# Kernel optimization log

Hardware: AMD Instinct MI355X
Metric: run time of the kernel (lower is better)

The kernel has to match this reference:

```python
import jax, jax.numpy as jnp
import numpy as np

B, T, C = 4, 4096, 1024
H, CS = 16, 128
D = C // H
EPS = 1e-5

def _ln(x, g, b):
    m = jnp.mean(x, axis=-1, keepdims=True)
    v = jnp.var(x, axis=-1, keepdims=True)
    return (x - m) * jax.lax.rsqrt(v + EPS) * g + b

def setup_inputs() -> dict:
    key = jax.random.key(0)
    ks = jax.random.split(key, 12)
    s_c = 1.0 / np.sqrt(C)
    s_2d = 1.0 / np.sqrt(2 * D)
    return {
        "x": jax.random.normal(ks[0], (B, T, C), jnp.float32),
        "mark_W": jax.random.normal(ks[1], (C, C), jnp.float32) * s_c,
        "mark_b": jnp.zeros((C,), jnp.float32),
        "gate_W": jax.random.normal(ks[2], (C, C), jnp.float32) * s_c,
        "gate_b": jnp.zeros((C,), jnp.float32),
        "carry_g": jnp.ones((D,), jnp.float32),
        "carry_b": jnp.zeros((D,), jnp.float32),
        "card_g": jnp.ones((D,), jnp.float32),
        "card_b": jnp.zeros((D,), jnp.float32),
        "ho1_W": jax.random.normal(ks[3], (2 * D, 2 * D), jnp.float32) * s_2d,
        "ho1_b": jnp.zeros((2 * D,), jnp.float32),
        "ho2_W": jax.random.normal(ks[4], (2 * D, D), jnp.float32) * s_2d,
        "ho2_b": jnp.zeros((D,), jnp.float32),
        "proj_W": jax.random.normal(ks[5], (C, C), jnp.float32) * s_c * 0.02,
        "proj_b": jnp.zeros((C,), jnp.float32),
        "ln_g": jnp.ones((C,), jnp.float32),
        "ln_b": jnp.zeros((C,), jnp.float32),
    }

def reference(x, mark_W, mark_b, gate_W, gate_b, carry_g, carry_b,
              card_g, card_b, ho1_W, ho1_b, ho2_W, ho2_b,
              proj_W, proj_b, ln_g, ln_b):
    b, t, c = x.shape
    nc = t // CS  # T chosen divisible by chunk_size -> pad_len = 0
    pm = x @ mark_W + mark_b                       # [B,T,C]
    gates = jax.nn.sigmoid(x @ gate_W + gate_b)    # [B,T,C]

    def chunks(a):  # [B,T,C] -> [B,H,nc,CS,D]
        return a.reshape(b, nc, CS, H, D).transpose(0, 3, 1, 2, 4)

    x_h = chunks(x)
    gm = chunks(gates) * chunks(pm)                # gated marks
    lcm = jnp.cumsum(gm, axis=3)                   # local prefix sum within chunk
    chunk_sums = lcm[:, :, :, -1, :]               # [B,H,nc,D]
    carry_cum = jnp.cumsum(chunk_sums, axis=2)
    carries = jnp.concatenate(
        [jnp.zeros((b, H, 1, D), x.dtype), carry_cum[:, :, :-1, :]], axis=2)
    nrm_carry = _ln(carries, carry_g, carry_b)[:, :, :, None, :]  # [B,H,nc,1,D]
    mwc = lcm + nrm_carry                          # marks with carry
    cards_local = jnp.concatenate([nrm_carry, mwc[:, :, :, :-1, :]], axis=3)
    cards = _ln(cards_local, card_g, card_b)
    comb = jnp.concatenate([x_h, cards], axis=-1)  # [B,H,nc,CS,2D]
    h = jax.nn.gelu(comb @ ho1_W + ho1_b, approximate=False)
    ho = h @ ho2_W + ho2_b                         # [B,H,nc,CS,D]
    out = ho.transpose(0, 2, 3, 1, 4).reshape(b, t, c)
    out = out @ proj_W + proj_b
    out = _ln(out, ln_g, ln_b)
    return x + out
```

## Files before the change

kernel.cpp:

```cpp
#include <hip/hip_runtime.h>
#include <hip/hip_bf16.h>

typedef __bf16 bf16_t;
typedef __attribute__((ext_vector_type(8))) __bf16 bf16x8;
typedef __attribute__((ext_vector_type(4))) __bf16 bf16x4;
typedef __attribute__((ext_vector_type(4))) float f32x4;

static constexpr int Bn = 4, Tn = 4096, Cn = 1024, Hn = 16, CSn = 128, Dn = 64, NCn = 32;

#define DEVINL __device__ __forceinline__

DEVINL float wsum64(float v) {
  v += __shfl_xor(v, 32, 64);
  v += __shfl_xor(v, 16, 64);
  v += __shfl_xor(v, 8, 64);
  v += __shfl_xor(v, 4, 64);
  v += __shfl_xor(v, 2, 64);
  v += __shfl_xor(v, 1, 64);
  return v;
}

DEVINL float gelu_f(float v) {
  float x = v * 0.70710678f;
  float ax = fabsf(x);
  float t = 1.f / (1.f + 0.3275911f * ax);
  float poly = t * (0.254829592f +
               t * (-0.284496736f +
               t * (1.421413741f +
               t * (-1.453152027f +
               t * 1.061405429f))));
  float e = __expf(-ax * ax);
  float erfax = 1.f - poly * e;
  float erfx = copysignf(erfax, x);
  return 0.5f * v * (1.f + erfx);
}

DEVINL void gld16(const bf16_t* g, bf16_t* l) {
  __builtin_amdgcn_global_load_lds(
      (const __attribute__((address_space(1))) unsigned int*)(g),
      (__attribute__((address_space(3))) unsigned int*)(l), 16, 0, 0);
}

__global__ __launch_bounds__(256) void k_xbf(const float* __restrict__ in,
                                             bf16_t* __restrict__ out) {
  int i = blockIdx.x * 256 + threadIdx.x;
  float4 a = *reinterpret_cast<const float4*>(in + (size_t)i * 8);
  float4 b = *reinterpret_cast<const float4*>(in + (size_t)i * 8 + 4);
  bf16x8 o = {(bf16_t)a.x, (bf16_t)a.y, (bf16_t)a.z, (bf16_t)a.w,
              (bf16_t)b.x, (bf16_t)b.y, (bf16_t)b.z, (bf16_t)b.w};
  *reinterpret_cast<bf16x8*>(out + (size_t)i * 8) = o;
}

__global__ void k_transpose(const float* __restrict__ in, bf16_t* __restrict__ out,
                            int rows, int cols) {
  __shared__ float tile[64][65];
  int c0 = blockIdx.x * 64, r0 = blockIdx.y * 64;
  int tx = threadIdx.x & 63, ty = threadIdx.x >> 6;
#pragma unroll
  for (int i = ty; i < 64; i += 4)
    tile[i][tx] = in[(size_t)(r0 + i) * cols + c0 + tx];
  __syncthreads();
#pragma unroll
  for (int i = ty; i < 64; i += 4)
    out[(size_t)(c0 + i) * rows + r0 + tx] = (bf16_t)tile[tx][i];
}

__global__ __launch_bounds__(256, 2) void k_dualgemm_gm(
    const bf16_t* __restrict__ X, const bf16_t* __restrict__ Wtm,
    const bf16_t* __restrict__ Wtg, const float* __restrict__ bm,
    const float* __restrict__ bg, bf16_t* __restrict__ lcm,
    float* __restrict__ csum) {
  constexpr int K = Cn, N = Cn;
  constexpr int GP = 132;
  __shared__ __align__(16) bf16_t L[6][128 * 32];
  int tid = threadIdx.x;
  int Lb = blockIdx.x + 8 * blockIdx.y;
  int xcd = Lb & 7, jj = Lb >> 3;
  int nb = jj & 7, mb = xcd + 8 * (jj >> 3);
  int m0 = mb * 128, n0 = nb * 128;
  int wave = tid >> 6, lane = tid & 63;
  int wm = wave >> 1, wn = wave & 1;
  int lr = lane & 15, lk = lane >> 4;
  int rl = lane >> 2;
  int cl = (lane & 3) * 8;
  f32x4 accP[4][4] = {};
  f32x4 accG[4][4] = {};

  const bf16_t* Xb = X + (size_t)m0 * K;
  const bf16_t* Wmb = Wtm + (size_t)n0 * K;
  const bf16_t* Wgb = Wtg + (size_t)n0 * K;

#define STAGE3(buf, kt)                                                    \
  {                                                                        \
    _Pragma("unroll")                                                      \
    for (int c = 0; c < 2; ++c) {                                          \
      int ch = wave * 2 + c;                                               \
      size_t go = (size_t)(ch * 16 + rl) * K + (kt) * 32 + cl;             \
      int lo = ch * 512;                                                   \
      gld16(Xb + go, &L[0 + (buf)][lo]);                                   \
      gld16(Wmb + go, &L[2 + (buf)][lo]);                                  \
      gld16(Wgb + go, &L[4 + (buf)][lo]);                                  \
    }                                                                      \
  }

  STAGE3(0, 0);
  __syncthreads();
  int cur = 0;
  for (int kt = 0; kt < 32; ++kt) {
    if (kt < 31) STAGE3(cur ^ 1, kt + 1);
    bf16x8 af[4], bmf[4], bgf[4];
#pragma unroll
    for (int i = 0; i < 4; ++i)
      af[i] = *reinterpret_cast<const bf16x8*>(&L[0 + cur][(wm * 64 + i * 16 + lr) * 32 + lk * 8]);
#pragma unroll
    for (int j = 0; j < 4; ++j) {
      bmf[j] = *reinterpret_cast<const bf16x8*>(&L[2 + cur][(wn * 64 + j * 16 + lr) * 32 + lk * 8]);
      bgf[j] = *reinterpret_cast<const bf16x8*>(&L[4 + cur][(wn * 64 + j * 16 + lr) * 32 + lk * 8]);
    }
#pragma unroll
    for (int i = 0; i < 4; ++i)
#pragma unroll
      for (int j = 0; j < 4; ++j) {
        accP[i][j] = __builtin_amdgcn_mfma_f32_16x16x32_bf16(af[i], bmf[j], accP[i][j], 0, 0, 0);
        accG[i][j] = __builtin_amdgcn_mfma_f32_16x16x32_bf16(af[i], bgf[j], accG[i][j], 0, 0, 0);
      }
    __syncthreads();
    cur ^= 1;
  }
#undef STAGE3

  bf16_t* G = &L[0][0];
#pragma unroll
  for (int j = 0; j < 4; ++j) {
    int col = wn * 64 + j * 16 + lr;
    float bmv = bm[n0 + col], bgv = bg[n0 + col];
#pragma unroll
    for (int i = 0; i < 4; ++i) {
      int rbase = wm * 64 + i * 16 + lk * 4;
#pragma unroll
      for (int r = 0; r < 4; ++r) {
        float p = accP[i][j][r] + bmv;
        float g = accG[i][j][r] + bgv;
        float s = 1.f / (1.f + __expf(-g));
        G[(rbase + r) * GP + col] = (bf16_t)(s * p);
      }
    }
  }
  __syncthreads();
  if (tid < 128) {
    int col = tid;
    int bb = m0 >> 12;
    int ci = (m0 & 4095) >> 7;
    int gc = n0 + col;
    float run = 0.f;
    size_t obase = (size_t)m0 * N + gc;
#pragma unroll 8
    for (int pos = 0; pos < 128; ++pos) {
      run += (float)G[pos * GP + col];
      lcm[obase + (size_t)pos * N] = (bf16_t)run;
    }
    csum[(((size_t)bb * Hn + (gc >> 6)) * NCn + ci) * 64 + (gc & 63)] = run;
  }
}

__global__ __launch_bounds__(64) void k_carry_ln(const float* __restrict__ csum,
                                                 float* __restrict__ ncar,
                                                 const float* __restrict__ g,
                                                 const float* __restrict__ be) {
  int bh = blockIdx.x;
  int d = threadIdx.x;
  float gd = g[d], bd = be[d];
  float run = 0.f;
  for (int ci = 0; ci < NCn; ++ci) {
    float v = run;
    run += csum[((size_t)bh * NCn + ci) * 64 + d];
    float m = wsum64(v) * (1.f / 64.f);
    float dv = v - m;
    float var = wsum64(dv * dv) * (1.f / 64.f);
    ncar[((size_t)bh * NCn + ci) * 64 + d] = dv * rsqrtf(var + 1e-5f) * gd + bd;
  }
}

__global__ __launch_bounds__(256, 4) void k_ho_fused(
    const bf16_t* __restrict__ X, const bf16_t* __restrict__ lcm,
    const float* __restrict__ ncar, const float* __restrict__ cg,
    const float* __restrict__ cb, const bf16_t* __restrict__ W1t,
    const float* __restrict__ b1, const bf16_t* __restrict__ W2t,
    const float* __restrict__ b2, bf16_t* __restrict__ ho) {
  __shared__ __align__(16) bf16_t Cs[128][136];
  int tid = threadIdx.x;
  int ci = blockIdx.x & 31, bh = blockIdx.x >> 5;
  int h = bh & 15, b = bh >> 4;
  int wave = tid >> 6, lane = tid & 63;
  int wm = wave >> 1, wn = wave & 1;
  int lr = lane & 15, lk = lane >> 4;
  size_t xrow0 = (size_t)(b * Tn + ci * CSn);

  bf16x8 xf0[4], xf1[4];
#pragma unroll
  for (int i = 0; i < 4; ++i) {
    const bf16_t* xr = X + (xrow0 + wm * 64 + i * 16 + lr) * Cn + h * Dn + lk * 8;
    xf0[i] = *reinterpret_cast<const bf16x8*>(xr);
    xf1[i] = *reinterpret_cast<const bf16x8*>(xr + 32);
  }

  {
    int lg = lane >> 3;
    int le = lane & 7;
    int d0 = le * 8;
    const float* np = ncar + ((size_t)bh * NCn + ci) * 64 + d0;
    float ncv[8], ggv[8], bbv[8];
#pragma unroll
    for (int e = 0; e < 8; ++e) {
      ncv[e] = np[e];
      ggv[e] = cg[d0 + e];
      bbv[e] = cb[d0 + e];
    }
#pragma unroll
    for (int it = 0; it < 4; ++it) {
      int pr = wave * 32 + it * 8 + lg;
      float v[8];
      if (pr > 0) {
        bf16x8 lv = *reinterpret_cast<const bf16x8*>(
            lcm + (xrow0 + pr - 1) * Cn + h * Dn + d0);
#pragma unroll
        for (int e = 0; e < 8; ++e) v[e] = (float)lv[e] + ncv[e];
      } else {
#pragma unroll
        for (int e = 0; e < 8; ++e) v[e] = ncv[e];
      }
      float s = 0.f;
#pragma unroll
      for (int e = 0; e < 8; ++e) s += v[e];
      s += __shfl_xor(s, 1, 64);
      s += __shfl_xor(s, 2, 64);
      s += __shfl_xor(s, 4, 64);
      float mean = s * (1.f / 64.f);
      float q = 0.f;
#pragma unroll
      for (int e = 0; e < 8; ++e) { float dv = v[e] - mean; q += dv * dv; }
      q += __shfl_xor(q, 1, 64);
      q += __shfl_xor(q, 2, 64);
      q += __shfl_xor(q, 4, 64);
      float rs = rsqrtf(q * (1.f / 64.f) + 1e-5f);
      bf16x8 o;
#pragma unroll
      for (int e = 0; e < 8; ++e)
        o[e] = (bf16_t)((v[e] - mean) * rs * ggv[e] + bbv[e]);
      *reinterpret_cast<bf16x8*>(&Cs[pr][64 + d0]) = o;
    }
  }
  __syncthreads();
  f32x4 acc[4][4] = {};
#pragma unroll
  for (int ks = 0; ks < 4; ++ks) {
    bf16x8 af[4], bfr[4];
#pragma unroll
    for (int i = 0; i < 4; ++i) {
      if (ks == 0)      af[i] = xf0[i];
      else if (ks == 1) af[i] = xf1[i];
      else
        af[i] = *reinterpret_cast<const bf16x8*>(
            &Cs[wm * 64 + i * 16 + lr][64 + (ks - 2) * 32 + lk * 8]);
    }
#pragma unroll
    for (int j = 0; j < 4; ++j)
      bfr[j] = *reinterpret_cast<const bf16x8*>(
          W1t + (size_t)(wn * 64 + j * 16 + lr) * 128 + ks * 32 + lk * 8);
#pragma unroll
    for (int i = 0; i < 4; ++i)
#pragma unroll
      for (int j = 0; j < 4; ++j)
        acc[i][j] = __builtin_amdgcn_mfma_f32_16x16x32_bf16(af[i], bfr[j], acc[i][j], 0, 0, 0);
  }
  __syncthreads();
#pragma unroll
  for (int j = 0; j < 4; ++j) {
    int col = wn * 64 + j * 16 + lr;
    float bv = b1[col];
#pragma unroll
    for (int i = 0; i < 4; ++i) {
      int rbase = wm * 64 + i * 16 + lk * 4;
#pragma unroll
      for (int r = 0; r < 4; ++r)
        Cs[rbase + r][col] = (bf16_t)gelu_f(acc[i][j][r] + bv);
    }
  }
  __syncthreads();
  f32x4 acc2[2][4] = {};
#pragma unroll
  for (int ks = 0; ks < 4; ++ks) {
    bf16x8 af[2], bfr[4];
#pragma unroll
    for (int i = 0; i < 2; ++i)
      af[i] = *reinterpret_cast<const bf16x8*>(&Cs[wave * 32 + i * 16 + lr][ks * 32 + lk * 8]);
#pragma unroll
    for (int j = 0; j < 4; ++j)
      bfr[j] = *reinterpret_cast<const bf16x8*>(
          W2t + (size_t)(j * 16 + lr) * 128 + ks * 32 + lk * 8);
#pragma unroll
    for (int i = 0; i < 2; ++i)
#pragma unroll
      for (int j = 0; j < 4; ++j)
        acc2[i][j] = __builtin_amdgcn_mfma_f32_16x16x32_bf16(af[i], bfr[j], acc2[i][j], 0, 0, 0);
  }
#pragma unroll
  for (int j = 0; j < 4; ++j) {
    int dd = j * 16 + lr;
    float bv = b2[dd];
#pragma unroll
    for (int i = 0; i < 2; ++i) {
      int pbase = wave * 32 + i * 16 + lk * 4;
#pragma unroll
      for (int r = 0; r < 4; ++r)
        ho[(xrow0 + pbase + r) * Cn + h * Dn + dd] = (bf16_t)(acc2[i][j][r] + bv);
    }
  }
}

__global__ __launch_bounds__(256, 2) void k_gemm_bt(
    const bf16_t* __restrict__ A, const bf16_t* __restrict__ Wt,
    const float* __restrict__ bias, bf16_t* __restrict__ out) {
  constexpr int K = Cn, N = Cn;
  __shared__ __align__(16) bf16_t L[4][128 * 32];
  int tid = threadIdx.x;
  int Lb = blockIdx.x + 8 * blockIdx.y;
  int xcd = Lb & 7, jj = Lb >> 3;
  int nb = jj & 7, mb = xcd + 8 * (jj >> 3);
  int m0 = mb * 128, n0 = nb * 128;
  int wave = tid >> 6, lane = tid & 63;
  int wm = wave >> 1, wn = wave & 1;
  int lr = lane & 15, lk = lane >> 4;
  int rl = lane >> 2, cl = (lane & 3) * 8;
  f32x4 acc[4][4] = {};
  const bf16_t* Ab = A + (size_t)m0 * K;
  const bf16_t* Wb = Wt + (size_t)n0 * K;

#define STAGE2(buf, kt)                                                    \
  {                                                                        \
    _Pragma("unroll")                                                      \
    for (int c = 0; c < 2; ++c) {                                          \
      int ch = wave * 2 + c;                                               \
      size_t go = (size_t)(ch * 16 + rl) * K + (kt) * 32 + cl;             \
      int lo = ch * 512;                                                   \
      gld16(Ab + go, &L[0 + (buf)][lo]);                                   \
      gld16(Wb + go, &L[2 + (buf)][lo]);                                   \
    }                                                                      \
  }

  STAGE2(0, 0);
  __syncthreads();
  int cur = 0;
  for (int kt = 0; kt < 32; ++kt) {
    if (kt < 31) STAGE2(cur ^ 1, kt + 1);
    bf16x8 af[4], bfr[4];
#pragma unroll
    for (int i = 0; i < 4; ++i)
      af[i] = *reinterpret_cast<const bf16x8*>(&L[0 + cur][(wm * 64 + i * 16 + lr) * 32 + lk * 8]);
#pragma unroll
    for (int j = 0; j < 4; ++j)
      bfr[j] = *reinterpret_cast<const bf16x8*>(&L[2 + cur][(wn * 64 + j * 16 + lr) * 32 + lk * 8]);
#pragma unroll
    for (int i = 0; i < 4; ++i)
#pragma unroll
      for (int j = 0; j < 4; ++j)
        acc[i][j] = __builtin_amdgcn_mfma_f32_16x16x32_bf16(af[i], bfr[j], acc[i][j], 0, 0, 0);
    __syncthreads();
    cur ^= 1;
  }
#undef STAGE2
#pragma unroll
  for (int j = 0; j < 4; ++j) {
    int col = n0 + wn * 64 + j * 16 + lr;
    float bv = bias[col];
#pragma unroll
    for (int i = 0; i < 4; ++i) {
      int rbase = m0 + wm * 64 + i * 16 + lk * 4;
#pragma unroll
      for (int r = 0; r < 4; ++r)
        out[(size_t)(rbase + r) * N + col] = (bf16_t)(acc[i][j][r] + bv);
    }
  }
}

__global__ __launch_bounds__(256) void k_ln_residual(
    const bf16_t* __restrict__ pre, const float* __restrict__ X,
    const float* __restrict__ g, const float* __restrict__ be,
    float* __restrict__ out) {
  int row = blockIdx.x, t = threadIdx.x;
  size_t base = (size_t)row * Cn + t * 4;
  bf16x4 pv4 = *reinterpret_cast<const bf16x4*>(pre + base);
  float v0 = (float)pv4[0], v1 = (float)pv4[1], v2 = (float)pv4[2], v3 = (float)pv4[3];
  float s = v0 + v1 + v2 + v3;
  float q = v0 * v0 + v1 * v1 + v2 * v2 + v3 * v3;
  s = wsum64(s);
  q = wsum64(q);
  __shared__ float red[8];
  int wv = t >> 6, ln = t & 63;
  if (ln == 0) { red[wv] = s; red[4 + wv] = q; }
  __syncthreads();
  float tot = red[0] + red[1] + red[2] + red[3];
  float totq = red[4] + red[5] + red[6] + red[7];
  float mean = tot * (1.f / 1024.f);
  float var = totq * (1.f / 1024.f) - mean * mean;
  float rs = rsqrtf(fmaxf(var, 0.f) + 1e-5f);
  float4 xv = *reinterpret_cast<const float4*>(X + base);
  float4 gv = *reinterpret_cast<const float4*>(g + t * 4);
  float4 bv = *reinterpret_cast<const float4*>(be + t * 4);
  float4 o;
  o.x = (v0 - mean) * rs * gv.x + bv.x + xv.x;
  o.y = (v1 - mean) * rs * gv.y + bv.y + xv.y;
  o.z = (v2 - mean) * rs * gv.z + bv.z + xv.z;
  o.w = (v3 - mean) * rs * gv.w + bv.w + xv.w;
  *reinterpret_cast<float4*>(out + base) = o;
}

extern "C" void kernel_launch(void* const* d_in, const int* in_sizes, int n_in,
                              void* d_out, int out_size, void* d_ws, size_t ws_size,
                              hipStream_t stream) {
  const float* x       = (const float*)d_in[0];
  const float* mark_W  = (const float*)d_in[1];
  const float* mark_b  = (const float*)d_in[2];
  const float* gate_W  = (const float*)d_in[3];
  const float* gate_b  = (const float*)d_in[4];
  const float* carry_g = (const float*)d_in[5];
  const float* carry_b = (const float*)d_in[6];
  const float* card_g  = (const float*)d_in[7];
  const float* card_b  = (const float*)d_in[8];
  const float* ho1_W   = (const float*)d_in[9];
  const float* ho1_b   = (const float*)d_in[10];
  const float* ho2_W   = (const float*)d_in[11];
  const float* ho2_b   = (const float*)d_in[12];
  const float* proj_W  = (const float*)d_in[13];
  const float* proj_b  = (const float*)d_in[14];
  const float* ln_g    = (const float*)d_in[15];
  const float* ln_b    = (const float*)d_in[16];
  float* out = (float*)d_out;

  char* ws = (char*)d_ws;
  bf16_t* xbf    = (bf16_t*)(ws + 0);
  bf16_t* outpre = (bf16_t*)(ws + 0);
  bf16_t* gm     = (bf16_t*)(ws + 33554432);
  bf16_t* hobuf  = (bf16_t*)(ws + 100663296);
  float*  csum   = (float*)(ws + 134217728);
  float*  ncar   = (float*)(ws + 134742016);
  bf16_t* wtm    = (bf16_t*)(ws + 135266304);
  bf16_t* wtg    = (bf16_t*)(ws + 137363456);
  bf16_t* wtp    = (bf16_t*)(ws + 139460608);
  bf16_t* wt1    = (bf16_t*)(ws + 141557760);
  bf16_t* wt2    = (bf16_t*)(ws + 141590528);

  k_xbf<<<8192, 256, 0, stream>>>(x, xbf);
  k_transpose<<<dim3(16, 16), 256, 0, stream>>>(mark_W, wtm, 1024, 1024);
  k_transpose<<<dim3(16, 16), 256, 0, stream>>>(gate_W, wtg, 1024, 1024);
  k_transpose<<<dim3(16, 16), 256, 0, stream>>>(proj_W, wtp, 1024, 1024);
  k_transpose<<<dim3(2, 2),   256, 0, stream>>>(ho1_W, wt1, 128, 128);
  k_transpose<<<dim3(1, 2),   256, 0, stream>>>(ho2_W, wt2, 128, 64);

  k_dualgemm_gm<<<dim3(8, 128), 256, 0, stream>>>(xbf, wtm, wtg, mark_b, gate_b, gm, csum);
  k_carry_ln<<<64, 64, 0, stream>>>(csum, ncar, carry_g, carry_b);
  k_ho_fused<<<2048, 256, 0, stream>>>(xbf, gm, ncar, card_g, card_b,
                                       wt1, ho1_b, wt2, ho2_b, hobuf);
  k_gemm_bt<<<dim3(8, 128), 256, 0, stream>>>(hobuf, wtp, proj_b, outpre);
  k_ln_residual<<<16384, 256, 0, stream>>>(outpre, x, ln_g, ln_b, out);
}
```

Baseline: 258.3 us.

## Narrow dual-GEMM N tile to 64 and parallelise chunk prefix scan

The fused mark/gate GEMM moves from 128x128 to 128x64 output tiles, which halves the accumulator registers and shared memory so three blocks can share a CU and twice as many blocks launch. The epilogue cumsum over 128 rows now uses all 256 threads: each of four quarter-segments sums 32 rows, the offsets are combined through shared memory, and every thread then writes its own segment. The cost is that the X tile is reloaded twice as often, since each X panel now feeds only 64 output columns.

```diff
diff --git a/kernel.cpp b/kernel.cpp
--- a/kernel.cpp
+++ b/kernel.cpp
@@ -65,42 +65,46 @@
     out[(size_t)(c0 + i) * rows + r0 + tx] = (bf16_t)tile[tx][i];
 }
 
-__global__ __launch_bounds__(256, 2) void k_dualgemm_gm(
+__global__ __launch_bounds__(256, 3) void k_dualgemm_gm(
     const bf16_t* __restrict__ X, const bf16_t* __restrict__ Wtm,
     const bf16_t* __restrict__ Wtg, const float* __restrict__ bm,
     const float* __restrict__ bg, bf16_t* __restrict__ lcm,
     float* __restrict__ csum) {
   constexpr int K = Cn, N = Cn;
-  constexpr int GP = 132;
-  __shared__ __align__(16) bf16_t L[6][128 * 32];
+  constexpr int GP = 68;
+  __shared__ __align__(16) bf16_t L[16384];
+  __shared__ float tot[4][64];
   int tid = threadIdx.x;
-  int Lb = blockIdx.x + 8 * blockIdx.y;
+  int Lb = blockIdx.x;
   int xcd = Lb & 7, jj = Lb >> 3;
-  int nb = jj & 7, mb = xcd + 8 * (jj >> 3);
-  int m0 = mb * 128, n0 = nb * 128;
+  int nb = jj & 15, mb = xcd + 8 * (jj >> 4);
+  int m0 = mb * 128, n0 = nb * 64;
   int wave = tid >> 6, lane = tid & 63;
   int wm = wave >> 1, wn = wave & 1;
   int lr = lane & 15, lk = lane >> 4;
   int rl = lane >> 2;
   int cl = (lane & 3) * 8;
-  f32x4 accP[4][4] = {};
-  f32x4 accG[4][4] = {};
+  f32x4 accP[4][2] = {};
+  f32x4 accG[4][2] = {};
 
   const bf16_t* Xb = X + (size_t)m0 * K;
   const bf16_t* Wmb = Wtm + (size_t)n0 * K;
   const bf16_t* Wgb = Wtg + (size_t)n0 * K;
+  bf16_t* LA = L;
+  bf16_t* LBm = L + 8192;
+  bf16_t* LBg = L + 12288;
 
 #define STAGE3(buf, kt)                                                    \
   {                                                                        \
     _Pragma("unroll")                                                      \
     for (int c = 0; c < 2; ++c) {                                          \
       int ch = wave * 2 + c;                                               \
-      size_t go = (size_t)(ch * 16 + rl) * K + (kt) * 32 + cl;             \
-      int lo = ch * 512;                                                   \
-      gld16(Xb + go, &L[0 + (buf)][lo]);                                   \
-      gld16(Wmb + go, &L[2 + (buf)][lo]);                                  \
-      gld16(Wgb + go, &L[4 + (buf)][lo]);                                  \
+      gld16(Xb + (size_t)(ch * 16 + rl) * K + (kt) * 32 + cl,              \
+            LA + (buf) * 4096 + ch * 512);                                 \
     }                                                                      \
+    size_t gob = (size_t)(wave * 16 + rl) * K + (kt) * 32 + cl;            \
+    gld16(Wmb + gob, LBm + (buf) * 2048 + wave * 512);                     \
+    gld16(Wgb + gob, LBg + (buf) * 2048 + wave * 512);                     \
   }
 
   STAGE3(0, 0);
@@ -108,19 +112,22 @@
   int cur = 0;
   for (int kt = 0; kt < 32; ++kt) {
     if (kt < 31) STAGE3(cur ^ 1, kt + 1);
-    bf16x8 af[4], bmf[4], bgf[4];
+    bf16x8 af[4], bmf[2], bgf[2];
 #pragma unroll
     for (int i = 0; i < 4; ++i)
-      af[i] = *reinterpret_cast<const bf16x8*>(&L[0 + cur][(wm * 64 + i * 16 + lr) * 32 + lk * 8]);
-#pragma unroll
-    for (int j = 0; j < 4; ++j) {
-      bmf[j] = *reinterpret_cast<const bf16x8*>(&L[2 + cur][(wn * 64 + j * 16 + lr) * 32 + lk * 8]);
-      bgf[j] = *reinterpret_cast<const bf16x8*>(&L[4 + cur][(wn * 64 + j * 16 + lr) * 32 + lk * 8]);
+      af[i] = *reinterpret_cast<const bf16x8*>(
+          &LA[cur * 4096 + (wm * 64 + i * 16 + lr) * 32 + lk * 8]);
+#pragma unroll
+    for (int j = 0; j < 2; ++j) {
+      bmf[j] = *reinterpret_cast<const bf16x8*>(
+          &LBm[cur * 2048 + (wn * 32 + j * 16 + lr) * 32 + lk * 8]);
+      bgf[j] = *reinterpret_cast<const bf16x8*>(
+          &LBg[cur * 2048 + (wn * 32 + j * 16 + lr) * 32 + lk * 8]);
     }
 #pragma unroll
     for (int i = 0; i < 4; ++i)
 #pragma unroll
-      for (int j = 0; j < 4; ++j) {
+      for (int j = 0; j < 2; ++j) {
         accP[i][j] = __builtin_amdgcn_mfma_f32_16x16x32_bf16(af[i], bmf[j], accP[i][j], 0, 0, 0);
         accG[i][j] = __builtin_amdgcn_mfma_f32_16x16x32_bf16(af[i], bgf[j], accG[i][j], 0, 0, 0);
       }
@@ -129,10 +136,10 @@
   }
 #undef STAGE3
 
-  bf16_t* G = &L[0][0];
-#pragma unroll
-  for (int j = 0; j < 4; ++j) {
-    int col = wn * 64 + j * 16 + lr;
+  bf16_t* G = L;
+#pragma unroll
+  for (int j = 0; j < 2; ++j) {
+    int col = wn * 32 + j * 16 + lr;
     float bmv = bm[n0 + col], bgv = bg[n0 + col];
 #pragma unroll
     for (int i = 0; i < 4; ++i) {
@@ -147,19 +154,31 @@
     }
   }
   __syncthreads();
-  if (tid < 128) {
-    int col = tid;
-    int bb = m0 >> 12;
-    int ci = (m0 & 4095) >> 7;
+  {
+    int col = tid & 63;
+    int q = tid >> 6;
+    float lsum = 0.f;
+#pragma unroll 8
+    for (int r = 0; r < 32; ++r)
+      lsum += (float)G[(q * 32 + r) * GP + col];
+    tot[q][col] = lsum;
+    __syncthreads();
+    float run = 0.f;
+#pragma unroll
+    for (int qq = 0; qq < 3; ++qq)
+      if (qq < q) run += tot[qq][col];
     int gc = n0 + col;
-    float run = 0.f;
-    size_t obase = (size_t)m0 * N + gc;
+    size_t obase = (size_t)(m0 + q * 32) * N + gc;
 #pragma unroll 8
-    for (int pos = 0; pos < 128; ++pos) {
-      run += (float)G[pos * GP + col];
-      lcm[obase + (size_t)pos * N] = (bf16_t)run;
-    }
-    csum[(((size_t)bb * Hn + (gc >> 6)) * NCn + ci) * 64 + (gc & 63)] = run;
+    for (int r = 0; r < 32; ++r) {
+      run += (float)G[(q * 32 + r) * GP + col];
+      lcm[obase + (size_t)r * N] = (bf16_t)run;
+    }
+    if (q == 3) {
+      int bb = m0 >> 12;
+      int ci = (m0 >> 7) & 31;
+      csum[(((size_t)bb * Hn + (gc >> 6)) * NCn + ci) * 64 + (gc & 63)] = run;
+    }
   }
 }
 
@@ -457,7 +476,7 @@
   k_transpose<<<dim3(2, 2),   256, 0, stream>>>(ho1_W, wt1, 128, 128);
   k_transpose<<<dim3(1, 2),   256, 0, stream>>>(ho2_W, wt2, 128, 64);
 
-  k_dualgemm_gm<<<dim3(8, 128), 256, 0, stream>>>(xbf, wtm, wtg, mark_b, gate_b, gm, csum);
+  k_dualgemm_gm<<<2048, 256, 0, stream>>>(xbf, wtm, wtg, mark_b, gate_b, gm, csum);
   k_carry_ln<<<64, 64, 0, stream>>>(csum, ncar, carry_g, carry_b);
   k_ho_fused<<<2048, 256, 0, stream>>>(xbf, gm, ncar, card_g, card_b,
                                        wt1, ho1_b, wt2, ho2_b, hobuf);
```

Result: slower. 264.7 us (+2.5%).
